# Kernel optimization log

Hardware: AMD Instinct MI355X
Metric: run time of the kernel (lower is better)

The kernel has to match this reference:

```python
import jax, jax.numpy as jnp
import numpy as np

D_MODEL = 1024
N_HEADS = 16
D_HEAD = D_MODEL // N_HEADS
SPARSE_THRESH = 0.09
MASK_FILL = -1e9


def setup_inputs() -> dict:
    key = jax.random.key(0)
    ks = jax.random.split(key, 11)
    B, S, D = 4, 1024, D_MODEL
    # Xavier-uniform bound for square [D, D] linear weights
    bound = float(np.sqrt(6.0 / (D + D)))

    def xavier(k):
        return jax.random.uniform(k, (D, D), jnp.float32, -bound, bound)

    return {
        "q": jax.random.normal(ks[0], (B, S, D), jnp.float32),
        "k": jax.random.normal(ks[1], (B, S, D), jnp.float32),
        "v": jax.random.normal(ks[2], (B, S, D), jnp.float32),
        "Wq": xavier(ks[3]), "bq": jnp.zeros((D,), jnp.float32),
        "Wk": xavier(ks[4]), "bk": jnp.zeros((D,), jnp.float32),
        "Wv": xavier(ks[5]), "bv": jnp.zeros((D,), jnp.float32),
        "Wo": xavier(ks[6]), "bo": jnp.zeros((D,), jnp.float32),
    }


def reference(q, k, v, Wq, bq, Wk, bk, Wv, bv, Wo, bo):
    B, S, D = q.shape
    H, dk = N_HEADS, D_HEAD

    def proj(x, W, b):
        # nn.Linear: x @ W^T + b, then split heads -> [B, H, S, dk]
        y = jnp.einsum("bsd,ed->bse", x, W) + b
        return y.reshape(B, S, H, dk).transpose(0, 2, 1, 3)

    qh = proj(q, Wq, bq)
    kh = proj(k, Wk, bk)
    vh = proj(v, Wv, bv)

    scale = 1.0 / jnp.sqrt(jnp.asarray(dk, q.dtype))
    scores = jnp.einsum("bhqd,bhkd->bhqk", qh, kh) * scale  # [B,H,S,S]

    att1 = jax.nn.softmax(scores, axis=-1)
    # mask entries whose first-pass probability is below the sparsity threshold
    scores2 = jnp.where(att1 < SPARSE_THRESH, jnp.asarray(MASK_FILL, scores.dtype), scores)
    att2 = jax.nn.softmax(scores2, axis=-1)
    # dropout(p=0.2) is identity in eval mode (deterministic reference)

    ctx = jnp.einsum("bhqk,bhkd->bhqd", att2, vh)           # [B,H,S,dk]
    ctx = ctx.transpose(0, 2, 1, 3).reshape(B, S, D)
    return jnp.einsum("bsd,ed->bse", ctx, Wo) + bo
```

## Files before the change

### kernel.cpp

```cpp
#include <hip/hip_runtime.h>
#include <hip/hip_bf16.h>
#include <math.h>


constexpr int D_MODEL = 1024;
constexpr int N_HEADS = 16;
constexpr int D_HEAD  = 64;
constexpr int SEQ     = 1024;
constexpr int BATCH   = 4;
constexpr float SPARSE_THRESH = 0.09f;

typedef short  bf16x8 __attribute__((ext_vector_type(8)));
typedef float  f32x4  __attribute__((ext_vector_type(4)));

__device__ __forceinline__ unsigned short f2bf_rne(float x) {
    unsigned u = __float_as_uint(x);
    u += 0x7FFFu + ((u >> 16) & 1u);
    return (unsigned short)(u >> 16);
}
__device__ __forceinline__ float bf2f(unsigned short b) {
    return __uint_as_float(((unsigned)b) << 16);
}

__device__ __forceinline__ unsigned cvt2(float a, float b) {
    __hip_bfloat162 p = __float22bfloat162_rn(make_float2(a, b));
    unsigned u; __builtin_memcpy(&u, &p, 4); return u;
}
__device__ __forceinline__ void split4(float x0, float x1, float x2, float x3,
                                       unsigned* hw, unsigned* lw) {
    const unsigned uh0 = cvt2(x0, x1);
    hw[0] = uh0;
    lw[0] = cvt2(x0 - __uint_as_float(uh0 << 16),
                 x1 - __uint_as_float(uh0 & 0xFFFF0000u));
    const unsigned uh1 = cvt2(x2, x3);
    hw[1] = uh1;
    lw[1] = cvt2(x2 - __uint_as_float(uh1 << 16),
                 x3 - __uint_as_float(uh1 & 0xFFFF0000u));
}

union BF8 { unsigned u[4]; bf16x8 v; };

__device__ __forceinline__ void unpack_pair(const unsigned* u, bf16x8& hi, bf16x8& lo) {
    BF8 h, l;
    #pragma unroll
    for (int p = 0; p < 4; ++p) {
        h.u[p] = (u[2 * p] >> 16)      | (u[2 * p + 1] & 0xFFFF0000u);
        l.u[p] = (u[2 * p] & 0xFFFFu)  | (u[2 * p + 1] << 16);
    }
    hi = h.v; lo = l.v;
}

__global__ __launch_bounds__(256)
void conv_w(const float* __restrict__ Wq, const float* __restrict__ Wk,
            const float* __restrict__ Wv,
            unsigned short* __restrict__ Wqh, unsigned short* __restrict__ Wql,
            unsigned short* __restrict__ Wkh, unsigned short* __restrict__ Wkl,
            unsigned short* __restrict__ Wvh, unsigned short* __restrict__ Wvl)
{
    const int NW8 = (D_MODEL * D_MODEL) / 8;
    int i = blockIdx.x * 256 + threadIdx.x;
    const float* s; unsigned short *dh, *dl;
    if (i < NW8)            { s = Wq; dh = Wqh; dl = Wql; }
    else if (i < 2 * NW8)   { i -= NW8; s = Wk; dh = Wkh; dl = Wkl; }
    else                    { i -= 2 * NW8; s = Wv; dh = Wvh; dl = Wvl; }
    const float4 x0 = ((const float4*)(s + (size_t)i * 8))[0];
    const float4 x1 = ((const float4*)(s + (size_t)i * 8))[1];
    unsigned hw[4], lw[4];
    split4(x0.x, x0.y, x0.z, x0.w, &hw[0], &lw[0]);
    split4(x1.x, x1.y, x1.z, x1.w, &hw[2], &lw[2]);
    *(uint4*)&dh[(size_t)i * 8] = *(const uint4*)hw;
    *(uint4*)&dl[(size_t)i * 8] = *(const uint4*)lw;
}

__global__ __launch_bounds__(256, 3)
void proj_qkv(const float* __restrict__ q, const float* __restrict__ k,
              const float* __restrict__ v,
              const unsigned short* __restrict__ Wqh, const unsigned short* __restrict__ Wql,
              const unsigned short* __restrict__ Wkh, const unsigned short* __restrict__ Wkl,
              const unsigned short* __restrict__ Wvh, const unsigned short* __restrict__ Wvl,
              const float* __restrict__ bq, const float* __restrict__ bk,
              const float* __restrict__ bv,
              unsigned* __restrict__ qp, unsigned* __restrict__ kp,
              unsigned short* __restrict__ vt)
{
    __shared__ unsigned short SM[4][128][40];
    unsigned short (*A_h)[40] = SM[0];
    unsigned short (*A_l)[40] = SM[1];
    unsigned short (*B_h)[40] = SM[2];
    unsigned short (*B_l)[40] = SM[3];

    const int z = blockIdx.z;
    const float* X    = (z == 0) ? q   : (z == 1) ? k   : v;
    const unsigned short* Wh = (z == 0) ? Wqh : (z == 1) ? Wkh : Wvh;
    const unsigned short* Wl = (z == 0) ? Wql : (z == 1) ? Wkl : Wvl;
    const float* bias = (z == 0) ? bq  : (z == 1) ? bk  : bv;
    const float scale = (z == 0) ? 0.125f : 1.0f;

    const int K = D_MODEL;
    const int tid = threadIdx.x, lane = tid & 63;
    const int l15 = lane & 15, l4 = lane >> 4;
    const int wv4 = tid >> 6;
    const int wr = (wv4 >> 1) * 64, wc = (wv4 & 1) * 64;
    const int bm = blockIdx.x * 128, bn = blockIdx.y * 128;
    const int sr = tid >> 1, sh = (tid & 1) * 16;

    f32x4 acc[4][4];
    #pragma unroll
    for (int i = 0; i < 4; ++i)
        #pragma unroll
        for (int j = 0; j < 4; ++j) acc[i][j] = (f32x4){0.f, 0.f, 0.f, 0.f};

    const float* ga = X + (size_t)(bm + sr) * K + sh;
    const unsigned short* gbh = Wh + (size_t)(bn + sr) * K + sh;
    const unsigned short* gbl = Wl + (size_t)(bn + sr) * K + sh;

    float4 av[4];
    uint4 wbh0, wbh1, wbl0, wbl1;
    #pragma unroll
    for (int l = 0; l < 4; ++l) av[l] = *(const float4*)&ga[l * 4];
    wbh0 = *(const uint4*)&gbh[0]; wbh1 = *(const uint4*)&gbh[8];
    wbl0 = *(const uint4*)&gbl[0]; wbl1 = *(const uint4*)&gbl[8];

    #pragma unroll 1
    for (int k0 = 0; k0 < K; k0 += 32) {
        unsigned ahw[8], alw[8];
        #pragma unroll
        for (int l = 0; l < 4; ++l)
            split4(av[l].x, av[l].y, av[l].z, av[l].w, &ahw[l * 2], &alw[l * 2]);

        __syncthreads();
        *(uint4*)&A_h[sr][sh]     = *(const uint4*)&ahw[0];
        *(uint4*)&A_h[sr][sh + 8] = *(const uint4*)&ahw[4];
        *(uint4*)&A_l[sr][sh]     = *(const uint4*)&alw[0];
        *(uint4*)&A_l[sr][sh + 8] = *(const uint4*)&alw[4];
        *(uint4*)&B_h[sr][sh]     = wbh0;
        *(uint4*)&B_h[sr][sh + 8] = wbh1;
        *(uint4*)&B_l[sr][sh]     = wbl0;
        *(uint4*)&B_l[sr][sh + 8] = wbl1;
        __syncthreads();

        if (k0 + 32 < K) {
            const int o = k0 + 32;
            #pragma unroll
            for (int l = 0; l < 4; ++l) av[l] = *(const float4*)&ga[o + l * 4];
            wbh0 = *(const uint4*)&gbh[o]; wbh1 = *(const uint4*)&gbh[o + 8];
            wbl0 = *(const uint4*)&gbl[o]; wbl1 = *(const uint4*)&gbl[o + 8];
        }

        bf16x8 ah[4], al4[4], bh4[4], bl4[4];
        #pragma unroll
        for (int i = 0; i < 4; ++i) {
            const int r = wr + i * 16 + l15;
            const int c = wc + i * 16 + l15;
            ah[i]  = *(const bf16x8*)&A_h[r][l4 * 8];
            al4[i] = *(const bf16x8*)&A_l[r][l4 * 8];
            bh4[i] = *(const bf16x8*)&B_h[c][l4 * 8];
            bl4[i] = *(const bf16x8*)&B_l[c][l4 * 8];
        }
        #pragma unroll
        for (int i = 0; i < 4; ++i)
            #pragma unroll
            for (int j = 0; j < 4; ++j) {
                acc[i][j] = __builtin_amdgcn_mfma_f32_16x16x32_bf16(ah[i],  bh4[j], acc[i][j], 0, 0, 0);
                acc[i][j] = __builtin_amdgcn_mfma_f32_16x16x32_bf16(ah[i],  bl4[j], acc[i][j], 0, 0, 0);
                acc[i][j] = __builtin_amdgcn_mfma_f32_16x16x32_bf16(al4[i], bh4[j], acc[i][j], 0, 0, 0);
            }
    }

    if (z == 2) {
        unsigned short* T = &SM[0][0][0];
        __syncthreads();
        #pragma unroll
        for (int i = 0; i < 4; ++i)
            #pragma unroll
            for (int j = 0; j < 4; ++j) {
                const int cl = wc + j * 16 + l15;
                const int sl = wr + i * 16 + l4 * 4;
                const float bi = bias[bn + cl];
                unsigned short h4[4];
                #pragma unroll
                for (int r = 0; r < 4; ++r)
                    h4[r] = f2bf_rne(acc[i][j][r] + bi);
                *(uint2*)&T[cl * 136 + sl] = *(const uint2*)&h4[0];
            }
        __syncthreads();
        const int c = tid >> 1, half = tid & 1;
        const int bb = bm >> 10;
        const int sb = (bm & (SEQ - 1)) + half * 64;
        unsigned short* dst = vt + (((size_t)bb << 20) + (size_t)(bn + c) * SEQ + sb);
        const unsigned short* srcT = &T[c * 136 + half * 64];
        #pragma unroll
        for (int u = 0; u < 8; ++u)
            *(uint4*)&dst[u * 8] = *(const uint4*)&srcT[u * 8];
        return;
    }

    unsigned* Cp = (z == 0) ? qp : kp;
    #pragma unroll
    for (int i = 0; i < 4; ++i)
        #pragma unroll
        for (int j = 0; j < 4; ++j) {
            const int rb = bm + wr + i * 16 + l4 * 4;
            const int c  = bn + wc + j * 16 + l15;
            const float bi = bias[c];
            const int h = c >> 6, d = c & (D_HEAD - 1);
            #pragma unroll
            for (int r = 0; r < 4; ++r) {
                const float val = (acc[i][j][r] + bi) * scale;
                const unsigned short hu = f2bf_rne(val);
                const unsigned short lu = f2bf_rne(val - bf2f(hu));
                const int mrow = rb + r;
                const int b = mrow >> 10, s = mrow & (SEQ - 1);
                Cp[((size_t)(b * N_HEADS + h) * SEQ + s) * D_HEAD + d] =
                    ((unsigned)hu << 16) | lu;
            }
        }
}

__global__ __launch_bounds__(256, 3)
void proj_o(const unsigned short* __restrict__ Act, const float* __restrict__ W,
            const float* __restrict__ bias, float* __restrict__ out)
{
    __shared__ unsigned short A_h[128][40];
    __shared__ unsigned short B_h[128][40];

    const int K = D_MODEL;
    const int tid = threadIdx.x, lane = tid & 63;
    const int l15 = lane & 15, l4 = lane >> 4;
    const int wv4 = tid >> 6;
    const int wr = (wv4 >> 1) * 64, wc = (wv4 & 1) * 64;
    const int bm = blockIdx.x * 128, bn = blockIdx.y * 128;
    const int sr = tid >> 1, sh = (tid & 1) * 16;

    f32x4 acc[4][4];
    #pragma unroll
    for (int i = 0; i < 4; ++i)
        #pragma unroll
        for (int j = 0; j < 4; ++j) acc[i][j] = (f32x4){0.f, 0.f, 0.f, 0.f};

    const unsigned short* ga = Act + (size_t)(bm + sr) * K + sh;
    const float* gb = W + (size_t)(bn + sr) * K + sh;

    uint4 av0 = *(const uint4*)&ga[0], av1 = *(const uint4*)&ga[8];
    float4 bv4[4];
    #pragma unroll
    for (int l = 0; l < 4; ++l) bv4[l] = *(const float4*)&gb[l * 4];

    #pragma unroll 1
    for (int k0 = 0; k0 < K; k0 += 32) {
        unsigned bhw[8];
        #pragma unroll
        for (int l = 0; l < 4; ++l) {
            bhw[l * 2]     = cvt2(bv4[l].x, bv4[l].y);
            bhw[l * 2 + 1] = cvt2(bv4[l].z, bv4[l].w);
        }

        __syncthreads();
        *(uint4*)&A_h[sr][sh]     = av0;
        *(uint4*)&A_h[sr][sh + 8] = av1;
        *(uint4*)&B_h[sr][sh]     = *(const uint4*)&bhw[0];
        *(uint4*)&B_h[sr][sh + 8] = *(const uint4*)&bhw[4];
        __syncthreads();

        if (k0 + 32 < K) {
            av0 = *(const uint4*)&ga[k0 + 32];
            av1 = *(const uint4*)&ga[k0 + 32 + 8];
            #pragma unroll
            for (int l = 0; l < 4; ++l)
                bv4[l] = *(const float4*)&gb[k0 + 32 + l * 4];
        }

        bf16x8 ah[4], bh4[4];
        #pragma unroll
        for (int i = 0; i < 4; ++i) {
            ah[i]  = *(const bf16x8*)&A_h[wr + i * 16 + l15][l4 * 8];
            bh4[i] = *(const bf16x8*)&B_h[wc + i * 16 + l15][l4 * 8];
        }
        #pragma unroll
        for (int i = 0; i < 4; ++i)
            #pragma unroll
            for (int j = 0; j < 4; ++j)
                acc[i][j] = __builtin_amdgcn_mfma_f32_16x16x32_bf16(ah[i], bh4[j], acc[i][j], 0, 0, 0);
    }

    #pragma unroll
    for (int i = 0; i < 4; ++i)
        #pragma unroll
        for (int j = 0; j < 4; ++j) {
            const int rb = bm + wr + i * 16 + l4 * 4;
            const int c  = bn + wc + j * 16 + l15;
            const float bi = bias[c];
            #pragma unroll
            for (int r = 0; r < 4; ++r)
                out[(size_t)(rb + r) * D_MODEL + c] = acc[i][j][r] + bi;
        }
}

__device__ __forceinline__ void score_from_lds(
    const unsigned short (* __restrict__ KH)[72], const unsigned short (* __restrict__ KL)[72],
    int l15, int l4, const bf16x8 (&qh)[2][2], const bf16x8 (&ql)[2][2], f32x4 acc[2][4])
{
    #pragma unroll
    for (int j = 0; j < 4; ++j) {
        const int row = l15 + 16 * j;
        const bf16x8 kh0 = *(const bf16x8*)&KH[row][l4 * 8];
        const bf16x8 kh1 = *(const bf16x8*)&KH[row][32 + l4 * 8];
        const bf16x8 kl0 = *(const bf16x8*)&KL[row][l4 * 8];
        const bf16x8 kl1 = *(const bf16x8*)&KL[row][32 + l4 * 8];
        #pragma unroll
        for (int st = 0; st < 2; ++st) {
            f32x4 a = (f32x4){0.f, 0.f, 0.f, 0.f};
            a = __builtin_amdgcn_mfma_f32_16x16x32_bf16(qh[st][0], kh0, a, 0, 0, 0);
            a = __builtin_amdgcn_mfma_f32_16x16x32_bf16(qh[st][0], kl0, a, 0, 0, 0);
            a = __builtin_amdgcn_mfma_f32_16x16x32_bf16(ql[st][0], kh0, a, 0, 0, 0);
            a = __builtin_amdgcn_mfma_f32_16x16x32_bf16(qh[st][1], kh1, a, 0, 0, 0);
            a = __builtin_amdgcn_mfma_f32_16x16x32_bf16(qh[st][1], kl1, a, 0, 0, 0);
            a = __builtin_amdgcn_mfma_f32_16x16x32_bf16(ql[st][1], kh1, a, 0, 0, 0);
            acc[st][j] = a;
        }
    }
}

__global__ __launch_bounds__(256, 3)
void attn_mfma(const unsigned* __restrict__ qp, const unsigned* __restrict__ kp,
               const unsigned short* __restrict__ vt, unsigned short* __restrict__ ctxh)
{
    __shared__ unsigned short KHL[2][2][64][72];
    __shared__ unsigned short Wl[4][32][64];
    __shared__ float Vm[64];
    __shared__ int AnyNU;
    float (*Pm)[4] = (float (*)[4])&Wl[0][0][0];

    const int tid  = threadIdx.x;
    const int lane = tid & 63;
    const int wv   = tid >> 6;
    const int l15  = lane & 15, l4 = lane >> 4;
    const int bh   = blockIdx.x;
    const int b    = bh >> 4, h = bh & 15;
    const int q0   = blockIdx.y * 128 + wv * 32;

    bf16x8 qh[2][2], ql[2][2];
    #pragma unroll
    for (int st = 0; st < 2; ++st) {
        const unsigned* qrow = qp + ((size_t)bh * SEQ + q0 + st * 16 + l15) * D_HEAD;
        #pragma unroll
        for (int ks = 0; ks < 2; ++ks) {
            unsigned u[8];
            *(uint4*)&u[0] = *(const uint4*)&qrow[ks * 32 + l4 * 8];
            *(uint4*)&u[4] = *(const uint4*)&qrow[ks * 32 + l4 * 8 + 4];
            unpack_pair(u, qh[st][ks], ql[st][ks]);
        }
    }

    const unsigned short* vtb = vt + (size_t)bh * D_HEAD * SEQ;

    {
        const int d = tid >> 2, q4 = tid & 3;
        const unsigned short* vr = vtb + (size_t)d * SEQ + q4 * 256;
        float s0 = 0.f, s1 = 0.f, s2 = 0.f, s3 = 0.f;
        #pragma unroll 4
        for (int i = 0; i < 32; ++i) {
            bf16x8 v8 = *(const bf16x8*)&vr[i * 8];
            s0 += bf2f((unsigned short)v8[0]) + bf2f((unsigned short)v8[4]);
            s1 += bf2f((unsigned short)v8[1]) + bf2f((unsigned short)v8[5]);
            s2 += bf2f((unsigned short)v8[2]) + bf2f((unsigned short)v8[6]);
            s3 += bf2f((unsigned short)v8[3]) + bf2f((unsigned short)v8[7]);
        }
        Pm[d][q4] = (s0 + s1) + (s2 + s3);
        if (tid == 0) AnyNU = 0;
    }

    const int sr = tid >> 2;
    const int sd = (tid & 3) * 16;
    const unsigned* kpb = kp + (size_t)bh * SEQ * D_HEAD;

    {
        unsigned u[16];
        const unsigned* src = kpb + (size_t)sr * D_HEAD + sd;
        #pragma unroll
        for (int g = 0; g < 4; ++g) *(uint4*)&u[g * 4] = *(const uint4*)&src[g * 4];
        bf16x8 h0, l0, h1, l1;
        unpack_pair(&u[0], h0, l0);
        unpack_pair(&u[8], h1, l1);
        *(bf16x8*)&KHL[0][0][sr][sd]     = h0;
        *(bf16x8*)&KHL[0][0][sr][sd + 8] = h1;
        *(bf16x8*)&KHL[0][1][sr][sd]     = l0;
        *(bf16x8*)&KHL[0][1][sr][sd + 8] = l1;
    }
    __syncthreads();

    if (tid < 64)
        Vm[tid] = (Pm[tid][0] + Pm[tid][1] + Pm[tid][2] + Pm[tid][3]) * (1.f / 1024.f);

    float mloc[2][4], zloc[2][4];
    #pragma unroll
    for (int st = 0; st < 2; ++st)
        #pragma unroll
        for (int r = 0; r < 4; ++r) { mloc[st][r] = -1e30f; zloc[st][r] = 0.f; }

    int cur = 0;

    #pragma unroll 1
    for (int c = 0; c < 16; ++c) {
        unsigned u[16];
        const int cn = (c + 1) & 15;
        const unsigned* src = kpb + ((size_t)cn * 64 + sr) * D_HEAD + sd;
        #pragma unroll
        for (int g = 0; g < 4; ++g) *(uint4*)&u[g * 4] = *(const uint4*)&src[g * 4];

        f32x4 acc[2][4];
        score_from_lds(KHL[cur][0], KHL[cur][1], l15, l4, qh, ql, acc);

        #pragma unroll
        for (int st = 0; st < 2; ++st)
            #pragma unroll
            for (int r = 0; r < 4; ++r) {
                const float a0 = acc[st][0][r], a1 = acc[st][1][r];
                const float a2 = acc[st][2][r], a3 = acc[st][3][r];
                mloc[st][r] = fmaxf(mloc[st][r], fmaxf(fmaxf(a0, a1), fmaxf(a2, a3)));
                zloc[st][r] += (__expf(a0) + __expf(a1)) + (__expf(a2) + __expf(a3));
            }

        bf16x8 h0, l0, h1, l1;
        unpack_pair(&u[0], h0, l0);
        unpack_pair(&u[8], h1, l1);
        const int nxt = cur ^ 1;
        *(bf16x8*)&KHL[nxt][0][sr][sd]     = h0;
        *(bf16x8*)&KHL[nxt][0][sr][sd + 8] = h1;
        *(bf16x8*)&KHL[nxt][1][sr][sd]     = l0;
        *(bf16x8*)&KHL[nxt][1][sr][sd + 8] = l1;
        __syncthreads();
        cur = nxt;
    }

    float taue[2][4];
    bool  unif[2][4];
    int mynu = 0;
    #pragma unroll
    for (int st = 0; st < 2; ++st)
        #pragma unroll
        for (int r = 0; r < 4; ++r) {
            float mm = mloc[st][r], zz = zloc[st][r];
            #pragma unroll
            for (int o = 1; o <= 8; o <<= 1) {
                mm = fmaxf(mm, __shfl_xor(mm, o, 16));
                zz += __shfl_xor(zz, o, 16);
            }
            const float tau = __logf(SPARSE_THRESH * zz);
            const bool uni = (mm < tau);
            unif[st][r] = uni;
            taue[st][r] = uni ? 3.0e38f : tau;
            mynu |= uni ? 0 : 1;
        }
    if (__any(mynu)) { if (lane == 0) atomicOr(&AnyNU, 1); }
    __syncthreads();
    const bool runB = (AnyNU != 0);

    float z2[2][4];
    f32x4 pv[2][4];
    #pragma unroll
    for (int st = 0; st < 2; ++st)
        #pragma unroll
        for (int r = 0; r < 4; ++r) { z2[st][r] = 0.f; pv[st][r] = (f32x4){0.f, 0.f, 0.f, 0.f}; }

    if (runB) {
        #pragma unroll 1
        for (int c = 0; c < 16; ++c) {
            unsigned u[16];
            const int cn = (c + 1) & 15;
            const unsigned* src = kpb + ((size_t)cn * 64 + sr) * D_HEAD + sd;
            #pragma unroll
            for (int g = 0; g < 4; ++g) *(uint4*)&u[g * 4] = *(const uint4*)&src[g * 4];

            f32x4 acc[2][4];
            score_from_lds(KHL[cur][0], KHL[cur][1], l15, l4, qh, ql, acc);

            int any = 0;
            #pragma unroll
            for (int st = 0; st < 2; ++st)
                #pragma unroll
                for (int r = 0; r < 4; ++r) {
                    const float rmax = fmaxf(fmaxf(acc[st][0][r], acc[st][1][r]),
                                             fmaxf(acc[st][2][r], acc[st][3][r]));
                    any |= (rmax >= taue[st][r]) ? 1 : 0;
                }

            if (__any(any)) {
                #pragma unroll
                for (int st = 0; st < 2; ++st)
                    #pragma unroll
                    for (int j = 0; j < 4; ++j)
                        #pragma unroll
                        for (int r = 0; r < 4; ++r) {
                            const float a = acc[st][j][r];
                            const float w = (a >= taue[st][r]) ? __expf(a) : 0.f;
                            const unsigned short wb = f2bf_rne(w);
                            z2[st][r] += bf2f(wb);
                            Wl[wv][st * 16 + l4 * 4 + r][l15 + 16 * j] = wb;
                        }
                asm volatile("s_waitcnt lgkmcnt(0)" ::: "memory");
                __builtin_amdgcn_sched_barrier(0);

                bf16x8 wa[2][2];
                #pragma unroll
                for (int st = 0; st < 2; ++st)
                    #pragma unroll
                    for (int ks = 0; ks < 2; ++ks)
                        wa[st][ks] = *(const bf16x8*)&Wl[wv][st * 16 + l15][ks * 32 + l4 * 8];

                #pragma unroll
                for (int ds = 0; ds < 4; ++ds) {
                    const bf16x8 v0 = *(const bf16x8*)
                        &vtb[(size_t)(ds * 16 + l15) * SEQ + c * 64 + l4 * 8];
                    const bf16x8 v1 = *(const bf16x8*)
                        &vtb[(size_t)(ds * 16 + l15) * SEQ + c * 64 + 32 + l4 * 8];
                    #pragma unroll
                    for (int st = 0; st < 2; ++st) {
                        pv[st][ds] = __builtin_amdgcn_mfma_f32_16x16x32_bf16(wa[st][0], v0, pv[st][ds], 0, 0, 0);
                        pv[st][ds] = __builtin_amdgcn_mfma_f32_16x16x32_bf16(wa[st][1], v1, pv[st][ds], 0, 0, 0);
                    }
                }
            }

            bf16x8 h0, l0, h1, l1;
            unpack_pair(&u[0], h0, l0);
            unpack_pair(&u[8], h1, l1);
            const int nxt = cur ^ 1;
            *(bf16x8*)&KHL[nxt][0][sr][sd]     = h0;
            *(bf16x8*)&KHL[nxt][0][sr][sd + 8] = h1;
            *(bf16x8*)&KHL[nxt][1][sr][sd]     = l0;
            *(bf16x8*)&KHL[nxt][1][sr][sd + 8] = l1;
            __syncthreads();
            cur = nxt;
        }

        #pragma unroll
        for (int st = 0; st < 2; ++st)
            #pragma unroll
            for (int r = 0; r < 4; ++r) {
                #pragma unroll
                for (int o = 1; o <= 8; o <<= 1) z2[st][r] += __shfl_xor(z2[st][r], o, 16);
            }
    }

    float* Tw = (float*)&KHL[0][0][0][0] + wv * 2176;
    #pragma unroll
    for (int st = 0; st < 2; ++st)
        #pragma unroll
        for (int r = 0; r < 4; ++r) {
            const float inv = unif[st][r] ? 0.f : (1.f / z2[st][r]);
            const int row = st * 16 + l4 * 4 + r;
            #pragma unroll
            for (int ds = 0; ds < 4; ++ds) {
                const int d = ds * 16 + l15;
                Tw[row * 68 + d] = unif[st][r] ? Vm[d] : pv[st][ds][r] * inv;
            }
        }
    asm volatile("s_waitcnt lgkmcnt(0)" ::: "memory");
    __builtin_amdgcn_sched_barrier(0);

    const int rr = lane >> 1, seg = lane & 1;
    const size_t gbase = ((size_t)b * SEQ + q0 + rr) * D_MODEL + h * D_HEAD + seg * 32;
    #pragma unroll
    for (int u2 = 0; u2 < 8; ++u2) {
        const float4 t = *(const float4*)&Tw[rr * 68 + seg * 32 + u2 * 4];
        unsigned short h4[4] = {f2bf_rne(t.x), f2bf_rne(t.y), f2bf_rne(t.z), f2bf_rne(t.w)};
        *(uint2*)&ctxh[gbase + u2 * 4] = *(const uint2*)h4;
    }
}

extern "C" void kernel_launch(void* const* d_in, const int* in_sizes, int n_in,
                              void* d_out, int out_size, void* d_ws, size_t ws_size,
                              hipStream_t stream)
{
    const float* q  = (const float*)d_in[0];
    const float* k  = (const float*)d_in[1];
    const float* v  = (const float*)d_in[2];
    const float* Wq = (const float*)d_in[3];
    const float* bq = (const float*)d_in[4];
    const float* Wk = (const float*)d_in[5];
    const float* bk = (const float*)d_in[6];
    const float* Wv = (const float*)d_in[7];
    const float* bv = (const float*)d_in[8];
    const float* Wo = (const float*)d_in[9];
    const float* bo = (const float*)d_in[10];
    float* out = (float*)d_out;

    const size_t MB = 1 << 20;
    char* w = (char*)d_ws;
    unsigned* qp = (unsigned*)(w);
    unsigned* kp = (unsigned*)(w + 16 * MB);
    unsigned short* vt   = (unsigned short*)(w + 32 * MB);
    unsigned short* ctxh = (unsigned short*)(w + 40 * MB);
    unsigned short* Wqh = (unsigned short*)(w + 48 * MB);
    unsigned short* Wql = (unsigned short*)(w + 50 * MB);
    unsigned short* Wkh = (unsigned short*)(w + 52 * MB);
    unsigned short* Wkl = (unsigned short*)(w + 54 * MB);
    unsigned short* Wvh = (unsigned short*)(w + 56 * MB);
    unsigned short* Wvl = (unsigned short*)(w + 58 * MB);

    const int NW8 = (D_MODEL * D_MODEL) / 8;

    conv_w<<<(3 * NW8) / 256, 256, 0, stream>>>(Wq, Wk, Wv, Wqh, Wql, Wkh, Wkl, Wvh, Wvl);

    proj_qkv<<<dim3(32, 8, 3), 256, 0, stream>>>(q, k, v,
                                                 Wqh, Wql, Wkh, Wkl, Wvh, Wvl,
                                                 bq, bk, bv, qp, kp, vt);

    attn_mfma<<<dim3(BATCH * N_HEADS, SEQ / 128), 256, 0, stream>>>(qp, kp, vt, ctxh);

    proj_o<<<dim3(32, 8), 256, 0, stream>>>(ctxh, Wo, bo, out);
}
```

Measured before the change: 178.2 us.

## Split attention block into 8 waves of 16 query rows each

The attention kernel now launches 512 threads per block, and each wave handles 16 query rows instead of 32. The K staging, V-mean partial sums and output store are re-partitioned across the 8 waves. The goal is more waves per CU and shorter per-wave dependency chains, which helps hide latency in the serial score and exp loops. In exchange each wave reuses every K tile loaded from LDS for half as many rows, so LDS read traffic per useful MFMA doubles, and the block-wide syncs now wait on more waves.

```diff
diff --git a/kernel.cpp b/kernel.cpp
--- a/kernel.cpp
+++ b/kernel.cpp
@@ -296,9 +296,9 @@
         }
 }
 
-__device__ __forceinline__ void score_from_lds(
+__device__ __forceinline__ void score16(
     const unsigned short (* __restrict__ KH)[72], const unsigned short (* __restrict__ KL)[72],
-    int l15, int l4, const bf16x8 (&qh)[2][2], const bf16x8 (&ql)[2][2], f32x4 acc[2][4])
+    int l15, int l4, const bf16x8 (&qh)[2], const bf16x8 (&ql)[2], f32x4 acc[4])
 {
     #pragma unroll
     for (int j = 0; j < 4; ++j) {
@@ -307,29 +307,26 @@
         const bf16x8 kh1 = *(const bf16x8*)&KH[row][32 + l4 * 8];
         const bf16x8 kl0 = *(const bf16x8*)&KL[row][l4 * 8];
         const bf16x8 kl1 = *(const bf16x8*)&KL[row][32 + l4 * 8];
-        #pragma unroll
-        for (int st = 0; st < 2; ++st) {
-            f32x4 a = (f32x4){0.f, 0.f, 0.f, 0.f};
-            a = __builtin_amdgcn_mfma_f32_16x16x32_bf16(qh[st][0], kh0, a, 0, 0, 0);
-            a = __builtin_amdgcn_mfma_f32_16x16x32_bf16(qh[st][0], kl0, a, 0, 0, 0);
-            a = __builtin_amdgcn_mfma_f32_16x16x32_bf16(ql[st][0], kh0, a, 0, 0, 0);
-            a = __builtin_amdgcn_mfma_f32_16x16x32_bf16(qh[st][1], kh1, a, 0, 0, 0);
-            a = __builtin_amdgcn_mfma_f32_16x16x32_bf16(qh[st][1], kl1, a, 0, 0, 0);
-            a = __builtin_amdgcn_mfma_f32_16x16x32_bf16(ql[st][1], kh1, a, 0, 0, 0);
-            acc[st][j] = a;
-        }
-    }
-}
-
-__global__ __launch_bounds__(256, 3)
+        f32x4 a = (f32x4){0.f, 0.f, 0.f, 0.f};
+        a = __builtin_amdgcn_mfma_f32_16x16x32_bf16(qh[0], kh0, a, 0, 0, 0);
+        a = __builtin_amdgcn_mfma_f32_16x16x32_bf16(qh[0], kl0, a, 0, 0, 0);
+        a = __builtin_amdgcn_mfma_f32_16x16x32_bf16(ql[0], kh0, a, 0, 0, 0);
+        a = __builtin_amdgcn_mfma_f32_16x16x32_bf16(qh[1], kh1, a, 0, 0, 0);
+        a = __builtin_amdgcn_mfma_f32_16x16x32_bf16(qh[1], kl1, a, 0, 0, 0);
+        a = __builtin_amdgcn_mfma_f32_16x16x32_bf16(ql[1], kh1, a, 0, 0, 0);
+        acc[j] = a;
+    }
+}
+
+__global__ __launch_bounds__(512, 4)
 void attn_mfma(const unsigned* __restrict__ qp, const unsigned* __restrict__ kp,
                const unsigned short* __restrict__ vt, unsigned short* __restrict__ ctxh)
 {
     __shared__ unsigned short KHL[2][2][64][72];
-    __shared__ unsigned short Wl[4][32][64];
+    __shared__ unsigned short Wl[8][16][64];
     __shared__ float Vm[64];
     __shared__ int AnyNU;
-    float (*Pm)[4] = (float (*)[4])&Wl[0][0][0];
+    float (*Pm)[8] = (float (*)[8])&Wl[0][0][0];
 
     const int tid  = threadIdx.x;
     const int lane = tid & 63;
@@ -337,176 +334,156 @@
     const int l15  = lane & 15, l4 = lane >> 4;
     const int bh   = blockIdx.x;
     const int b    = bh >> 4, h = bh & 15;
-    const int q0   = blockIdx.y * 128 + wv * 32;
-
-    bf16x8 qh[2][2], ql[2][2];
-    #pragma unroll
-    for (int st = 0; st < 2; ++st) {
-        const unsigned* qrow = qp + ((size_t)bh * SEQ + q0 + st * 16 + l15) * D_HEAD;
+    const int q0   = blockIdx.y * 128 + wv * 16;
+
+    bf16x8 qh[2], ql[2];
+    {
+        const unsigned* qrow = qp + ((size_t)bh * SEQ + q0 + l15) * D_HEAD;
         #pragma unroll
         for (int ks = 0; ks < 2; ++ks) {
             unsigned u[8];
             *(uint4*)&u[0] = *(const uint4*)&qrow[ks * 32 + l4 * 8];
             *(uint4*)&u[4] = *(const uint4*)&qrow[ks * 32 + l4 * 8 + 4];
-            unpack_pair(u, qh[st][ks], ql[st][ks]);
+            unpack_pair(u, qh[ks], ql[ks]);
         }
     }
 
     const unsigned short* vtb = vt + (size_t)bh * D_HEAD * SEQ;
 
     {
-        const int d = tid >> 2, q4 = tid & 3;
-        const unsigned short* vr = vtb + (size_t)d * SEQ + q4 * 256;
+        const int d = tid >> 3, q8 = tid & 7;
+        const unsigned short* vr = vtb + (size_t)d * SEQ + q8 * 128;
         float s0 = 0.f, s1 = 0.f, s2 = 0.f, s3 = 0.f;
         #pragma unroll 4
-        for (int i = 0; i < 32; ++i) {
+        for (int i = 0; i < 16; ++i) {
             bf16x8 v8 = *(const bf16x8*)&vr[i * 8];
             s0 += bf2f((unsigned short)v8[0]) + bf2f((unsigned short)v8[4]);
             s1 += bf2f((unsigned short)v8[1]) + bf2f((unsigned short)v8[5]);
             s2 += bf2f((unsigned short)v8[2]) + bf2f((unsigned short)v8[6]);
             s3 += bf2f((unsigned short)v8[3]) + bf2f((unsigned short)v8[7]);
         }
-        Pm[d][q4] = (s0 + s1) + (s2 + s3);
+        Pm[d][q8] = (s0 + s1) + (s2 + s3);
         if (tid == 0) AnyNU = 0;
     }
 
-    const int sr = tid >> 2;
-    const int sd = (tid & 3) * 16;
+    const int sr = tid >> 3;
+    const int sd = (tid & 7) * 8;
     const unsigned* kpb = kp + (size_t)bh * SEQ * D_HEAD;
 
     {
-        unsigned u[16];
+        unsigned u[8];
         const unsigned* src = kpb + (size_t)sr * D_HEAD + sd;
-        #pragma unroll
-        for (int g = 0; g < 4; ++g) *(uint4*)&u[g * 4] = *(const uint4*)&src[g * 4];
-        bf16x8 h0, l0, h1, l1;
-        unpack_pair(&u[0], h0, l0);
-        unpack_pair(&u[8], h1, l1);
-        *(bf16x8*)&KHL[0][0][sr][sd]     = h0;
-        *(bf16x8*)&KHL[0][0][sr][sd + 8] = h1;
-        *(bf16x8*)&KHL[0][1][sr][sd]     = l0;
-        *(bf16x8*)&KHL[0][1][sr][sd + 8] = l1;
+        *(uint4*)&u[0] = *(const uint4*)&src[0];
+        *(uint4*)&u[4] = *(const uint4*)&src[4];
+        bf16x8 h0, l0;
+        unpack_pair(u, h0, l0);
+        *(bf16x8*)&KHL[0][0][sr][sd] = h0;
+        *(bf16x8*)&KHL[0][1][sr][sd] = l0;
     }
     __syncthreads();
 
     if (tid < 64)
-        Vm[tid] = (Pm[tid][0] + Pm[tid][1] + Pm[tid][2] + Pm[tid][3]) * (1.f / 1024.f);
-
-    float mloc[2][4], zloc[2][4];
-    #pragma unroll
-    for (int st = 0; st < 2; ++st)
-        #pragma unroll
-        for (int r = 0; r < 4; ++r) { mloc[st][r] = -1e30f; zloc[st][r] = 0.f; }
+        Vm[tid] = (((Pm[tid][0] + Pm[tid][1]) + (Pm[tid][2] + Pm[tid][3]))
+                 + ((Pm[tid][4] + Pm[tid][5]) + (Pm[tid][6] + Pm[tid][7]))) * (1.f / 1024.f);
+
+    float mloc[4], zloc[4];
+    #pragma unroll
+    for (int r = 0; r < 4; ++r) { mloc[r] = -1e30f; zloc[r] = 0.f; }
 
     int cur = 0;
 
     #pragma unroll 1
     for (int c = 0; c < 16; ++c) {
-        unsigned u[16];
+        unsigned u[8];
         const int cn = (c + 1) & 15;
         const unsigned* src = kpb + ((size_t)cn * 64 + sr) * D_HEAD + sd;
-        #pragma unroll
-        for (int g = 0; g < 4; ++g) *(uint4*)&u[g * 4] = *(const uint4*)&src[g * 4];
-
-        f32x4 acc[2][4];
-        score_from_lds(KHL[cur][0], KHL[cur][1], l15, l4, qh, ql, acc);
-
-        #pragma unroll
-        for (int st = 0; st < 2; ++st)
-            #pragma unroll
-            for (int r = 0; r < 4; ++r) {
-                const float a0 = acc[st][0][r], a1 = acc[st][1][r];
-                const float a2 = acc[st][2][r], a3 = acc[st][3][r];
-                mloc[st][r] = fmaxf(mloc[st][r], fmaxf(fmaxf(a0, a1), fmaxf(a2, a3)));
-                zloc[st][r] += (__expf(a0) + __expf(a1)) + (__expf(a2) + __expf(a3));
-            }
-
-        bf16x8 h0, l0, h1, l1;
-        unpack_pair(&u[0], h0, l0);
-        unpack_pair(&u[8], h1, l1);
+        *(uint4*)&u[0] = *(const uint4*)&src[0];
+        *(uint4*)&u[4] = *(const uint4*)&src[4];
+
+        f32x4 acc[4];
+        score16(KHL[cur][0], KHL[cur][1], l15, l4, qh, ql, acc);
+
+        #pragma unroll
+        for (int r = 0; r < 4; ++r) {
+            const float a0 = acc[0][r], a1 = acc[1][r];
+            const float a2 = acc[2][r], a3 = acc[3][r];
+            mloc[r] = fmaxf(mloc[r], fmaxf(fmaxf(a0, a1), fmaxf(a2, a3)));
+            zloc[r] += (__expf(a0) + __expf(a1)) + (__expf(a2) + __expf(a3));
+        }
+
+        bf16x8 h0, l0;
+        unpack_pair(u, h0, l0);
         const int nxt = cur ^ 1;
-        *(bf16x8*)&KHL[nxt][0][sr][sd]     = h0;
-        *(bf16x8*)&KHL[nxt][0][sr][sd + 8] = h1;
-        *(bf16x8*)&KHL[nxt][1][sr][sd]     = l0;
-        *(bf16x8*)&KHL[nxt][1][sr][sd + 8] = l1;
+        *(bf16x8*)&KHL[nxt][0][sr][sd] = h0;
+        *(bf16x8*)&KHL[nxt][1][sr][sd] = l0;
         __syncthreads();
         cur = nxt;
     }
 
-    float taue[2][4];
-    bool  unif[2][4];
+    float taue[4];
+    bool  unif[4];
     int mynu = 0;
     #pragma unroll
-    for (int st = 0; st < 2; ++st)
-        #pragma unroll
-        for (int r = 0; r < 4; ++r) {
-            float mm = mloc[st][r], zz = zloc[st][r];
-            #pragma unroll
-            for (int o = 1; o <= 8; o <<= 1) {
-                mm = fmaxf(mm, __shfl_xor(mm, o, 16));
-                zz += __shfl_xor(zz, o, 16);
-            }
-            const float tau = __logf(SPARSE_THRESH * zz);
-            const bool uni = (mm < tau);
-            unif[st][r] = uni;
-            taue[st][r] = uni ? 3.0e38f : tau;
-            mynu |= uni ? 0 : 1;
-        }
+    for (int r = 0; r < 4; ++r) {
+        float mm = mloc[r], zz = zloc[r];
+        #pragma unroll
+        for (int o = 1; o <= 8; o <<= 1) {
+            mm = fmaxf(mm, __shfl_xor(mm, o, 16));
+            zz += __shfl_xor(zz, o, 16);
+        }
+        const float tau = __logf(SPARSE_THRESH * zz);
+        const bool uni = (mm < tau);
+        unif[r] = uni;
+        taue[r] = uni ? 3.0e38f : tau;
+        mynu |= uni ? 0 : 1;
+    }
     if (__any(mynu)) { if (lane == 0) atomicOr(&AnyNU, 1); }
     __syncthreads();
     const bool runB = (AnyNU != 0);
 
-    float z2[2][4];
-    f32x4 pv[2][4];
-    #pragma unroll
-    for (int st = 0; st < 2; ++st)
-        #pragma unroll
-        for (int r = 0; r < 4; ++r) { z2[st][r] = 0.f; pv[st][r] = (f32x4){0.f, 0.f, 0.f, 0.f}; }
+    float z2[4];
+    f32x4 pv[4];
+    #pragma unroll
+    for (int r = 0; r < 4; ++r) { z2[r] = 0.f; pv[r] = (f32x4){0.f, 0.f, 0.f, 0.f}; }
 
     if (runB) {
         #pragma unroll 1
         for (int c = 0; c < 16; ++c) {
-            unsigned u[16];
+            unsigned u[8];
             const int cn = (c + 1) & 15;
             const unsigned* src = kpb + ((size_t)cn * 64 + sr) * D_HEAD + sd;
-            #pragma unroll
-            for (int g = 0; g < 4; ++g) *(uint4*)&u[g * 4] = *(const uint4*)&src[g * 4];
-
-            f32x4 acc[2][4];
-            score_from_lds(KHL[cur][0], KHL[cur][1], l15, l4, qh, ql, acc);
+            *(uint4*)&u[0] = *(const uint4*)&src[0];
+            *(uint4*)&u[4] = *(const uint4*)&src[4];
+
+            f32x4 acc[4];
+            score16(KHL[cur][0], KHL[cur][1], l15, l4, qh, ql, acc);
 
             int any = 0;
             #pragma unroll
-            for (int st = 0; st < 2; ++st)
-                #pragma unroll
-                for (int r = 0; r < 4; ++r) {
-                    const float rmax = fmaxf(fmaxf(acc[st][0][r], acc[st][1][r]),
-                                             fmaxf(acc[st][2][r], acc[st][3][r]));
-                    any |= (rmax >= taue[st][r]) ? 1 : 0;
-                }
+            for (int r = 0; r < 4; ++r) {
+                const float rmax = fmaxf(fmaxf(acc[0][r], acc[1][r]),
+                                         fmaxf(acc[2][r], acc[3][r]));
+                any |= (rmax >= taue[r]) ? 1 : 0;
+            }
 
             if (__any(any)) {
                 #pragma unroll
-                for (int st = 0; st < 2; ++st)
+                for (int j = 0; j < 4; ++j)
                     #pragma unroll
-                    for (int j = 0; j < 4; ++j)
-                        #pragma unroll
-                        for (int r = 0; r < 4; ++r) {
-                            const float a = acc[st][j][r];
-                            const float w = (a >= taue[st][r]) ? __expf(a) : 0.f;
-                            const unsigned short wb = f2bf_rne(w);
-                            z2[st][r] += bf2f(wb);
-                            Wl[wv][st * 16 + l4 * 4 + r][l15 + 16 * j] = wb;
-                        }
+                    for (int r = 0; r < 4; ++r) {
+                        const float a = acc[j][r];
+                        const float w = (a >= taue[r]) ? __expf(a) : 0.f;
+                        const unsigned short wb = f2bf_rne(w);
+                        z2[r] += bf2f(wb);
+                        Wl[wv][l4 * 4 + r][l15 + 16 * j] = wb;
+                    }
                 asm volatile("s_waitcnt lgkmcnt(0)" ::: "memory");
                 __builtin_amdgcn_sched_barrier(0);
 
-                bf16x8 wa[2][2];
+                bf16x8 wa[2];
                 #pragma unroll
-                for (int st = 0; st < 2; ++st)
-                    #pragma unroll
-                    for (int ks = 0; ks < 2; ++ks)
-                        wa[st][ks] = *(const bf16x8*)&Wl[wv][st * 16 + l15][ks * 32 + l4 * 8];
+                for (int ks = 0; ks < 2; ++ks)
+                    wa[ks] = *(const bf16x8*)&Wl[wv][l15][ks * 32 + l4 * 8];
 
                 #pragma unroll
                 for (int ds = 0; ds < 4; ++ds) {
@@ -514,56 +491,46 @@
                         &vtb[(size_t)(ds * 16 + l15) * SEQ + c * 64 + l4 * 8];
                     const bf16x8 v1 = *(const bf16x8*)
                         &vtb[(size_t)(ds * 16 + l15) * SEQ + c * 64 + 32 + l4 * 8];
-                    #pragma unroll
-                    for (int st = 0; st < 2; ++st) {
-                        pv[st][ds] = __builtin_amdgcn_mfma_f32_16x16x32_bf16(wa[st][0], v0, pv[st][ds], 0, 0, 0);
-                        pv[st][ds] = __builtin_amdgcn_mfma_f32_16x16x32_bf16(wa[st][1], v1, pv[st][ds], 0, 0, 0);
-                    }
+                    pv[ds] = __builtin_amdgcn_mfma_f32_16x16x32_bf16(wa[0], v0, pv[ds], 0, 0, 0);
+                    pv[ds] = __builtin_amdgcn_mfma_f32_16x16x32_bf16(wa[1], v1, pv[ds], 0, 0, 0);
                 }
             }
 
-            bf16x8 h0, l0, h1, l1;
-            unpack_pair(&u[0], h0, l0);
-            unpack_pair(&u[8], h1, l1);
+            bf16x8 h0, l0;
+            unpack_pair(u, h0, l0);
             const int nxt = cur ^ 1;
-            *(bf16x8*)&KHL[nxt][0][sr][sd]     = h0;
-            *(bf16x8*)&KHL[nxt][0][sr][sd + 8] = h1;
-            *(bf16x8*)&KHL[nxt][1][sr][sd]     = l0;
-            *(bf16x8*)&KHL[nxt][1][sr][sd + 8] = l1;
+            *(bf16x8*)&KHL[nxt][0][sr][sd] = h0;
+            *(bf16x8*)&KHL[nxt][1][sr][sd] = l0;
             __syncthreads();
             cur = nxt;
         }
 
         #pragma unroll
-        for (int st = 0; st < 2; ++st)
-            #pragma unroll
-            for (int r = 0; r < 4; ++r) {
-                #pragma unroll
-                for (int o = 1; o <= 8; o <<= 1) z2[st][r] += __shfl_xor(z2[st][r], o, 16);
-            }
-    }
-
-    float* Tw = (float*)&KHL[0][0][0][0] + wv * 2176;
-    #pragma unroll
-    for (int st = 0; st < 2; ++st)
-        #pragma unroll
         for (int r = 0; r < 4; ++r) {
-            const float inv = unif[st][r] ? 0.f : (1.f / z2[st][r]);
-            const int row = st * 16 + l4 * 4 + r;
-            #pragma unroll
-            for (int ds = 0; ds < 4; ++ds) {
-                const int d = ds * 16 + l15;
-                Tw[row * 68 + d] = unif[st][r] ? Vm[d] : pv[st][ds][r] * inv;
-            }
-        }
+            #pragma unroll
+            for (int o = 1; o <= 8; o <<= 1) z2[r] += __shfl_xor(z2[r], o, 16);
+        }
+    }
+
+    float* Tw = (float*)&KHL[0][0][0][0] + wv * 1088;
+    #pragma unroll
+    for (int r = 0; r < 4; ++r) {
+        const float inv = unif[r] ? 0.f : (1.f / z2[r]);
+        const int row = l4 * 4 + r;
+        #pragma unroll
+        for (int ds = 0; ds < 4; ++ds) {
+            const int d = ds * 16 + l15;
+            Tw[row * 68 + d] = unif[r] ? Vm[d] : pv[ds][r] * inv;
+        }
+    }
     asm volatile("s_waitcnt lgkmcnt(0)" ::: "memory");
     __builtin_amdgcn_sched_barrier(0);
 
-    const int rr = lane >> 1, seg = lane & 1;
-    const size_t gbase = ((size_t)b * SEQ + q0 + rr) * D_MODEL + h * D_HEAD + seg * 32;
-    #pragma unroll
-    for (int u2 = 0; u2 < 8; ++u2) {
-        const float4 t = *(const float4*)&Tw[rr * 68 + seg * 32 + u2 * 4];
+    const int rr = lane >> 2, seg = lane & 3;
+    const size_t gbase = ((size_t)b * SEQ + q0 + rr) * D_MODEL + h * D_HEAD + seg * 16;
+    #pragma unroll
+    for (int u2 = 0; u2 < 4; ++u2) {
+        const float4 t = *(const float4*)&Tw[rr * 68 + seg * 16 + u2 * 4];
         unsigned short h4[4] = {f2bf_rne(t.x), f2bf_rne(t.y), f2bf_rne(t.z), f2bf_rne(t.w)};
         *(uint2*)&ctxh[gbase + u2 * 4] = *(const uint2*)h4;
     }
@@ -607,7 +574,7 @@
                                                  Wqh, Wql, Wkh, Wkl, Wvh, Wvl,
                                                  bq, bk, bv, qp, kp, vt);
 
-    attn_mfma<<<dim3(BATCH * N_HEADS, SEQ / 128), 256, 0, stream>>>(qp, kp, vt, ctxh);
+    attn_mfma<<<dim3(BATCH * N_HEADS, SEQ / 128), 512, 0, stream>>>(qp, kp, vt, ctxh);
 
     proj_o<<<dim3(32, 8), 256, 0, stream>>>(ctxh, Wo, bo, out);
 }
```

Measured after the change: 175.4 us. No clear change (-1.6%).
